# Optimization experiments

Hardware: AMD Instinct MI355X
Metric: run time of the kernel (lower is better)

Reference implementation:

```python
import jax, jax.numpy as jnp
import numpy as np

N, E, DIN, DH, DOUT, H, G = 50000, 640000, 128, 64, 64, 4, 16

_PARAM_SHAPES = {
    "gat1_W": (DIN, H * DH), "gat1_asrc": (H, DH), "gat1_adst": (H, DH), "gat1_b": (DH,),
    "gat2_W": (DH, H * DH), "gat2_asrc": (H, DH), "gat2_adst": (H, DH), "gat2_b": (DH,),
    "gin_W1": (DH, DH), "gin_b1": (DH,), "gin_W2": (DH, DH), "gin_b2": (DH,),
    "sage1_Wl": (DH, DH), "sage1_bl": (DH,), "sage1_Wr": (DH, DH),
    "sage2_Wl": (DH, DH), "sage2_bl": (DH,), "sage2_Wr": (DH, DH),
    "tr_Wq": (DH, H * DH), "tr_bq": (H * DH,), "tr_Wk": (DH, H * DH), "tr_bk": (H * DH,),
    "tr_Wv": (DH, H * DH), "tr_bv": (H * DH,), "tr_Ws": (DH, DH), "tr_bs": (DH,),
    "ec_W1": (2 * DH, DH), "ec_b1": (DH,), "ec_W2": (DH, DH), "ec_b2": (DH,),
    "fc1_W": (DH, DH), "fc1_b": (DH,), "fc2_W": (DH, DOUT), "fc2_b": (DOUT,),
}
_PARAM_NAMES = list(_PARAM_SHAPES)


def setup_inputs() -> dict:
    key = jax.random.key(0)
    inp = {}
    inp["x"] = jax.random.normal(jax.random.fold_in(key, 0), (N, DIN), jnp.float32)
    inp["edge_index"] = jax.random.randint(jax.random.fold_in(key, 1), (2, E), 0, N, dtype=jnp.int32)
    inp["batch"] = jnp.sort(jax.random.randint(jax.random.fold_in(key, 2), (N,), 0, G, dtype=jnp.int32))
    for i, (name, shp) in enumerate(_PARAM_SHAPES.items()):
        inp[name] = jax.random.normal(jax.random.fold_in(key, 10 + i), shp, jnp.float32) * 0.05
    return inp


def _edge_softmax(logit, dst, n):
    # softmax over incoming edges of each target node (PyG scatter-softmax)
    m = jax.ops.segment_max(logit, dst, num_segments=n)
    e = jnp.exp(logit - m[dst])
    z = jax.ops.segment_sum(e, dst, num_segments=n)
    return e / (z[dst] + 1e-16)


def _forward(x, src, dst, batch, p):
    relu = jax.nn.relu
    # GATConv adds self-loops by default
    loop = jnp.arange(N, dtype=src.dtype)
    src_sl = jnp.concatenate([src, loop])
    dst_sl = jnp.concatenate([dst, loop])

    def gat(h_in, W, a_s, a_d, b):
        h = (h_in @ W).reshape(N, H, DH)                    # [N,H,D]
        ls = jnp.einsum('nhd,hd->nh', h, a_s)
        ld = jnp.einsum('nhd,hd->nh', h, a_d)
        logit = jax.nn.leaky_relu(ls[src_sl] + ld[dst_sl], 0.2)   # [E+N,H]
        alpha = _edge_softmax(logit, dst_sl, N)
        out = jax.ops.segment_sum(h[src_sl] * alpha[:, :, None], dst_sl, num_segments=N)
        return out.mean(axis=1) + b                          # concat=False -> head mean + bias

    x1 = relu(gat(x, p["gat1_W"], p["gat1_asrc"], p["gat1_adst"], p["gat1_b"]))
    x2 = relu(gat(x1, p["gat2_W"], p["gat2_asrc"], p["gat2_adst"], p["gat2_b"]))

    # GINConv: nn((1+eps)*x + sum_j x_j), eps=0
    agg = jax.ops.segment_sum(x2[src], dst, num_segments=N)
    x3 = relu(relu((x2 + agg) @ p["gin_W1"] + p["gin_b1"]) @ p["gin_W2"] + p["gin_b2"])

    deg = jax.ops.segment_sum(jnp.ones((E,), x.dtype), dst, num_segments=N)
    deg = jnp.maximum(deg, 1.0)[:, None]

    def sage(h_in, Wl, bl, Wr):
        mean = jax.ops.segment_sum(h_in[src], dst, num_segments=N) / deg
        return mean @ Wl + bl + h_in @ Wr

    xs = relu(sage(x3, p["sage1_Wl"], p["sage1_bl"], p["sage1_Wr"]))
    x4 = relu(sage(xs, p["sage2_Wl"], p["sage2_bl"], p["sage2_Wr"]))

    # TransformerConv (heads=4, concat=False, root_weight skip)
    q = (x4 @ p["tr_Wq"] + p["tr_bq"]).reshape(N, H, DH)
    k = (x4 @ p["tr_Wk"] + p["tr_bk"]).reshape(N, H, DH)
    v = (x4 @ p["tr_Wv"] + p["tr_bv"]).reshape(N, H, DH)
    logit = (q[dst] * k[src]).sum(-1) * (1.0 / np.sqrt(DH))  # [E,H]
    alpha = _edge_softmax(logit, dst, N)
    tout = jax.ops.segment_sum(v[src] * alpha[:, :, None], dst, num_segments=N).mean(axis=1)
    x5 = relu(tout + x4 @ p["tr_Ws"] + p["tr_bs"])

    # EdgeConv: max_j nn([x_i, x_j - x_i])
    xi = x5[dst]
    feat = jnp.concatenate([xi, x5[src] - xi], axis=1)       # [E, 2*DH]
    msg = relu(feat @ p["ec_W1"] + p["ec_b1"]) @ p["ec_W2"] + p["ec_b2"]
    emax = jax.ops.segment_max(msg, dst, num_segments=N)
    x6 = relu(jnp.where(jnp.isfinite(emax), emax, 0.0))      # isolated nodes -> 0

    # global_mean_pool over batch ids
    cnt = jax.ops.segment_sum(jnp.ones((N,), x.dtype), batch, num_segments=G)
    gmean = jax.ops.segment_sum(x6, batch, num_segments=G) / jnp.maximum(cnt, 1.0)[:, None]

    # dropout layers are identity in eval mode
    return relu(gmean @ p["fc1_W"] + p["fc1_b"]) @ p["fc2_W"] + p["fc2_b"]


def reference(x, edge_index, batch,
              gat1_W, gat1_asrc, gat1_adst, gat1_b,
              gat2_W, gat2_asrc, gat2_adst, gat2_b,
              gin_W1, gin_b1, gin_W2, gin_b2,
              sage1_Wl, sage1_bl, sage1_Wr,
              sage2_Wl, sage2_bl, sage2_Wr,
              tr_Wq, tr_bq, tr_Wk, tr_bk, tr_Wv, tr_bv, tr_Ws, tr_bs,
              ec_W1, ec_b1, ec_W2, ec_b2,
              fc1_W, fc1_b, fc2_W, fc2_b):
    L = dict(locals())
    p = {n: L[n] for n in _PARAM_NAMES}
    return _forward(x, edge_index[0], edge_index[1], batch, p)
```

## Files before the change

### kernel.cpp

```cpp
#include <hip/hip_runtime.h>

#define NN 50000
#define EE 640000
#define GG 16
#define N64 (NN*64)

static inline int cdiv(int a,int b){return (a+b-1)/b;}

typedef __attribute__((ext_vector_type(8))) short bfrag;
typedef __attribute__((ext_vector_type(4))) float ffrag;
typedef __attribute__((ext_vector_type(2))) float f32x2;

__device__ __forceinline__ float lrelu(float x){ return x>0.f? x : 0.2f*x; }
__device__ __forceinline__ unsigned fenc(float f){
  unsigned u=__float_as_uint(f);
  return (u&0x80000000u)? ~u : (u|0x80000000u);
}
__device__ __forceinline__ float bf2f(unsigned short u){ return __uint_as_float(((unsigned)u)<<16); }
__device__ __forceinline__ unsigned short f2bf(float f){
  unsigned u=__float_as_uint(f);
  u += 0x7FFFu + ((u>>16)&1u);
  return (unsigned short)(u>>16);
}
__device__ __forceinline__ unsigned char f2f8(float f){
  return (unsigned char)(__builtin_amdgcn_cvt_pk_fp8_f32(f,f,0,false)&0xff);
}
__device__ __forceinline__ void f8x4(unsigned u, float& e0,float& e1,float& e2,float& e3){
  f32x2 lo=__builtin_amdgcn_cvt_pk_f32_fp8((int)u,false);
  f32x2 hi=__builtin_amdgcn_cvt_pk_f32_fp8((int)u,true);
  e0=lo.x; e1=lo.y; e2=hi.x; e3=hi.y;
}
__device__ __forceinline__ float dot4f8(unsigned a, unsigned b){
  f32x2 al=__builtin_amdgcn_cvt_pk_f32_fp8((int)a,false);
  f32x2 ah=__builtin_amdgcn_cvt_pk_f32_fp8((int)a,true);
  f32x2 bl=__builtin_amdgcn_cvt_pk_f32_fp8((int)b,false);
  f32x2 bh=__builtin_amdgcn_cvt_pk_f32_fp8((int)b,true);
  return al.x*bl.x+al.y*bl.y+ah.x*bh.x+ah.y*bh.y;
}

__global__ void zero_kernel(unsigned* p, int n){
  int i=blockIdx.x*blockDim.x+threadIdx.x;
  if(i<n) p[i]=0u;
}

__global__ void hist_kernel(const int* __restrict__ dst, int* __restrict__ cnt){
  int e=blockIdx.x*blockDim.x+threadIdx.x;
  if(e<EE) atomicAdd(&cnt[dst[e]],1);
}

__global__ __launch_bounds__(1024) void scan1_kernel(const int* __restrict__ cnt,
    int* __restrict__ rowptr, int* __restrict__ bsum){
  __shared__ int wsum[16];
  int t=threadIdx.x, b=blockIdx.x;
  int i=b*1024+t;
  int v=(i<NN)?cnt[i]:0;
  int lane=t&63, w=t>>6;
  int inc=v;
  #pragma unroll
  for(int o=1;o<64;o<<=1){ int u=__shfl_up(inc,o,64); if(lane>=o) inc+=u; }
  if(lane==63) wsum[w]=inc;
  __syncthreads();
  if(t<16){
    int s=wsum[t];
    #pragma unroll
    for(int o=1;o<16;o<<=1){ int u=__shfl_up(s,o,16); if(t>=o) s+=u; }
    wsum[t]=s;
  }
  __syncthreads();
  int woff=(w>0)?wsum[w-1]:0;
  if(i<NN) rowptr[i]=woff+inc-v;
  if(t==1023) bsum[b]=wsum[15];
}

__global__ void scan2_kernel(const int* __restrict__ bsum, int* __restrict__ boff, int* __restrict__ rowptr, int nb){
  int t=threadIdx.x;
  int v=(t<nb)?bsum[t]:0;
  int inc=v;
  #pragma unroll
  for(int o=1;o<64;o<<=1){ int u=__shfl_up(inc,o,64); if(t>=o) inc+=u; }
  if(t<nb) boff[t]=inc-v;
  if(t==63) rowptr[NN]=inc;
}

__global__ void scan3_kernel(int* __restrict__ rowptr, const int* __restrict__ boff,
                             const int* __restrict__ cnt, float* __restrict__ invdeg){
  int i=blockIdx.x*blockDim.x+threadIdx.x;
  if(i<NN){
    rowptr[i]+=boff[i>>10];
    invdeg[i]=1.f/fmaxf((float)cnt[i],1.f);
  }
}

__global__ void fill_kernel(const int* __restrict__ src, const int* __restrict__ dst,
                            const int* __restrict__ rowptr, int* __restrict__ fillp,
                            int* __restrict__ srcS, int* __restrict__ dstS){
  int e=blockIdx.x*blockDim.x+threadIdx.x;
  if(e>=EE) return;
  int d=dst[e];
  int p=rowptr[d]+atomicAdd(&fillp[d],1);
  srcS[p]=src[e]; dstS[p]=d;
}

__global__ void cvtx_kernel(const float* __restrict__ x, unsigned short* __restrict__ xb){
  int i=blockIdx.x*blockDim.x+threadIdx.x;
  if(i>=NN*32) return;
  float4 v=*(const float4*)(x+(size_t)i*4);
  ushort4 o; o.x=f2bf(v.x); o.y=f2bf(v.y); o.z=f2bf(v.z); o.w=f2bf(v.w);
  *(ushort4*)(xb+(size_t)i*4)=o;
}

__global__ void prep_kernel(
    const float* __restrict__ g1W, const float* __restrict__ g2W,
    const float* __restrict__ giW1, const float* __restrict__ giW2,
    const float* __restrict__ s1Wl, const float* __restrict__ s1Wr,
    const float* __restrict__ s2Wl, const float* __restrict__ s2Wr,
    const float* __restrict__ Wq, const float* __restrict__ Wk,
    const float* __restrict__ Wv, const float* __restrict__ Ws,
    const float* __restrict__ ecW1, const float* __restrict__ ecW2,
    const float* __restrict__ bq, const float* __restrict__ bk, const float* __restrict__ eb1,
    unsigned short* __restrict__ wt, float* __restrict__ bqk, float* __restrict__ bPQ){
  int i=blockIdx.x*blockDim.x+threadIdx.x;
  if(i<32768){ int n=i>>7,k=i&127; wt[i]=f2bf(g1W[k*256+n]); return; } i-=32768;
  if(i<16384){ int n=i>>6,k=i&63; wt[32768+i]=f2bf(g2W[k*256+n]); return; } i-=16384;
  if(i<4096){ int n=i>>6,k=i&63; wt[49152+i]=f2bf(giW1[k*64+n]); return; } i-=4096;
  if(i<4096){ int n=i>>6,k=i&63; wt[53248+i]=f2bf(giW2[k*64+n]); return; } i-=4096;
  if(i<8192){ int n=i>>7,k=i&127; float v=(k<64)?s1Wl[k*64+n]:s1Wr[(k-64)*64+n];
              wt[57344+i]=f2bf(v); return; } i-=8192;
  if(i<8192){ int n=i>>7,k=i&127; float v=(k<64)?s2Wl[k*64+n]:s2Wr[(k-64)*64+n];
              wt[65536+i]=f2bf(v); return; } i-=8192;
  if(i<32768){ int n=i>>6,k=i&63; float v=(n<256)?Wq[k*256+n]:Wk[k*256+(n-256)];
               wt[73728+i]=f2bf(v); return; } i-=32768;
  if(i<16384){ int n=i>>6,k=i&63; wt[106496+i]=f2bf(Wv[k*256+n]); return; } i-=16384;
  if(i<4096){ int n=i>>6,k=i&63; wt[122880+i]=f2bf(Ws[k*64+n]); return; } i-=4096;
  if(i<8192){ int n=i>>6,k=i&63;
              float v=(n<64)?(ecW1[k*64+n]-ecW1[(64+k)*64+n]):ecW1[(64+k)*64+(n-64)];
              wt[126976+i]=f2bf(v); return; } i-=8192;
  if(i<4096){ int n=i>>6,k=i&63; wt[135168+i]=f2bf(ecW2[k*64+n]); return; } i-=4096;
  if(i<640){
    if(i<256) bqk[i]=bq[i];
    else if(i<512) bqk[i]=bk[i-256];
    else { int j=i-512; bPQ[j]=(j<64)?eb1[j]:0.f; }
  }
}

template<int K>
__global__ __launch_bounds__(256) void mgemm_kernel(
    const unsigned short* __restrict__ A, const unsigned short* __restrict__ Wt,
    const float* __restrict__ bias,
    float* __restrict__ Cf, unsigned short* __restrict__ Cb, unsigned char* __restrict__ C8,
    int ldc, int relu_flag, int c8dh,
    const float* __restrict__ a_s, const float* __restrict__ a_d,
    float* __restrict__ lsO, float* __restrict__ ldO){
  __shared__ float lsP[2][4][64];
  const int m0=blockIdx.x*64;
  const int tid=threadIdx.x;
  const int w=tid>>6, l=tid&63, lo=l&15, quad=l>>4;
  const int colg=blockIdx.y*64 + w*16 + lo;
  const unsigned short* wrow=Wt+(size_t)colg*K+quad*8;
  ffrag acc[4];
  #pragma unroll
  for(int t=0;t<4;t++) acc[t]=(ffrag){0.f,0.f,0.f,0.f};
  int rows[4];
  #pragma unroll
  for(int t=0;t<4;t++){ int r=m0+t*16+lo; rows[t]=(r<NN)?r:(NN-1); }
  #pragma unroll
  for(int kc=0;kc<K;kc+=32){
    bfrag b=*(const bfrag*)(wrow+kc);
    #pragma unroll
    for(int t=0;t<4;t++){
      bfrag a=*(const bfrag*)(A+(size_t)rows[t]*K+kc+quad*8);
      acc[t]=__builtin_amdgcn_mfma_f32_16x16x32_bf16(a,b,acc[t],0,0,0);
    }
  }
  float bv=bias?bias[colg]:0.f;
  float asv=0.f,adv=0.f;
  if(lsO){ asv=a_s[colg]; adv=a_d[colg]; }
  #pragma unroll
  for(int t=0;t<4;t++){
    #pragma unroll
    for(int r=0;r<4;r++){
      float v=acc[t][r]+bv;
      if(relu_flag) v=fmaxf(v,0.f);
      int row=m0+t*16+quad*4+r;
      if(row<NN){
        if(C8){ int ci=c8dh?(((colg&63)<<2)|(colg>>6)):colg; C8[(size_t)row*ldc+ci]=f2f8(v); }
        else if(Cb) Cb[(size_t)row*ldc+colg]=f2bf(v);
        else   Cf[(size_t)row*ldc+colg]=v;
      }
      if(lsO){
        float ps=v*asv, pd=v*adv;
        #pragma unroll
        for(int o=1;o<16;o<<=1){ ps+=__shfl_xor(ps,o,16); pd+=__shfl_xor(pd,o,16); }
        if(lo==0){ int lr=t*16+quad*4+r; lsP[0][w][lr]=ps; lsP[1][w][lr]=pd; }
      }
    }
  }
  if(lsO){
    __syncthreads();
    if(tid<64){
      int row=m0+tid;
      if(row<NN){
        lsO[(size_t)row*4+blockIdx.y]=lsP[0][0][tid]+lsP[0][1][tid]+lsP[0][2][tid]+lsP[0][3][tid];
        ldO[(size_t)row*4+blockIdx.y]=lsP[1][0][tid]+lsP[1][1][tid]+lsP[1][2][tid]+lsP[1][3][tid];
      }
    }
  }
}

__global__ __launch_bounds__(256) void gat1p_kernel(const unsigned char* __restrict__ h8,
    const int* __restrict__ rowptr, const int* __restrict__ srcS,
    const float* __restrict__ ls4, const float* __restrict__ ld4,
    const float* __restrict__ bias, unsigned short* __restrict__ outb){
  __shared__ float cz[4][4];
  __shared__ float ca[4][4][64];
  int w=threadIdx.x>>6, lane=threadIdx.x&63;
  int n=blockIdx.x*2+(w>>1);
  int half=w&1;
  float z0=0.f,z1=0.f,z2=0.f,z3=0.f;
  float a0=0.f,a1=0.f,a2=0.f,a3=0.f;
  if(n<NN){
    const float4 ldv=*(const float4*)(ld4+(size_t)4*n);
    int r0=rowptr[n], r1=rowptr[n+1];
    int mid=(r0+r1)>>1;
    if(half==0){
      const float4 lsv=*(const float4*)(ls4+(size_t)4*n);
      z0=__expf(lrelu(lsv.x+ldv.x)); z1=__expf(lrelu(lsv.y+ldv.y));
      z2=__expf(lrelu(lsv.z+ldv.z)); z3=__expf(lrelu(lsv.w+ldv.w));
      float h0,h1,h2,h3;
      f8x4(*(const unsigned*)(h8+(size_t)n*256+lane*4),h0,h1,h2,h3);
      a0=z0*h0; a1=z1*h1; a2=z2*h2; a3=z3*h3;
    }
    int j = half? mid : r0;
    int je= half? r1  : mid;
    for(; j+3<je; j+=4){
      int s0=srcS[j], s1=srcS[j+1], s2=srcS[j+2], s3=srcS[j+3];
      float4 L0=*(const float4*)(ls4+(size_t)4*s0);
      float4 L1=*(const float4*)(ls4+(size_t)4*s1);
      float4 L2=*(const float4*)(ls4+(size_t)4*s2);
      float4 L3=*(const float4*)(ls4+(size_t)4*s3);
      unsigned u0=*(const unsigned*)(h8+(size_t)s0*256+lane*4);
      unsigned u1=*(const unsigned*)(h8+(size_t)s1*256+lane*4);
      unsigned u2=*(const unsigned*)(h8+(size_t)s2*256+lane*4);
      unsigned u3=*(const unsigned*)(h8+(size_t)s3*256+lane*4);
      float E0x=__expf(lrelu(L0.x+ldv.x)),E0y=__expf(lrelu(L0.y+ldv.y)),
            E0z=__expf(lrelu(L0.z+ldv.z)),E0w=__expf(lrelu(L0.w+ldv.w));
      float E1x=__expf(lrelu(L1.x+ldv.x)),E1y=__expf(lrelu(L1.y+ldv.y)),
            E1z=__expf(lrelu(L1.z+ldv.z)),E1w=__expf(lrelu(L1.w+ldv.w));
      float E2x=__expf(lrelu(L2.x+ldv.x)),E2y=__expf(lrelu(L2.y+ldv.y)),
            E2z=__expf(lrelu(L2.z+ldv.z)),E2w=__expf(lrelu(L2.w+ldv.w));
      float E3x=__expf(lrelu(L3.x+ldv.x)),E3y=__expf(lrelu(L3.y+ldv.y)),
            E3z=__expf(lrelu(L3.z+ldv.z)),E3w=__expf(lrelu(L3.w+ldv.w));
      float h00,h01,h02,h03; f8x4(u0,h00,h01,h02,h03);
      float h10,h11,h12,h13; f8x4(u1,h10,h11,h12,h13);
      float h20,h21,h22,h23; f8x4(u2,h20,h21,h22,h23);
      float h30,h31,h32,h33; f8x4(u3,h30,h31,h32,h33);
      z0+=(E0x+E1x)+(E2x+E3x); z1+=(E0y+E1y)+(E2y+E3y);
      z2+=(E0z+E1z)+(E2z+E3z); z3+=(E0w+E1w)+(E2w+E3w);
      a0+=(E0x*h00+E1x*h10)+(E2x*h20+E3x*h30);
      a1+=(E0y*h01+E1y*h11)+(E2y*h21+E3y*h31);
      a2+=(E0z*h02+E1z*h12)+(E2z*h22+E3z*h32);
      a3+=(E0w*h03+E1w*h13)+(E2w*h23+E3w*h33);
    }
    for(; j<je; j++){
      int s0=srcS[j];
      float4 L0=*(const float4*)(ls4+(size_t)4*s0);
      unsigned u0=*(const unsigned*)(h8+(size_t)s0*256+lane*4);
      float E0x=__expf(lrelu(L0.x+ldv.x)),E0y=__expf(lrelu(L0.y+ldv.y)),
            E0z=__expf(lrelu(L0.z+ldv.z)),E0w=__expf(lrelu(L0.w+ldv.w));
      float h00,h01,h02,h03; f8x4(u0,h00,h01,h02,h03);
      z0+=E0x; z1+=E0y; z2+=E0z; z3+=E0w;
      a0+=E0x*h00; a1+=E0y*h01; a2+=E0z*h02; a3+=E0w*h03;
    }
  }
  if(lane==0){ cz[w][0]=z0; cz[w][1]=z1; cz[w][2]=z2; cz[w][3]=z3; }
  ca[w][0][lane]=a0; ca[w][1][lane]=a1; ca[w][2][lane]=a2; ca[w][3][lane]=a3;
  __syncthreads();
  if(threadIdx.x<128){
    int ni=threadIdx.x>>6, l=threadIdx.x&63;
    int n2=blockIdx.x*2+ni;
    if(n2<NN){
      int w0=ni*2, w1=w0+1;
      float Z0=cz[w0][0]+cz[w1][0], Z1=cz[w0][1]+cz[w1][1];
      float Z2=cz[w0][2]+cz[w1][2], Z3=cz[w0][3]+cz[w1][3];
      float A0=ca[w0][0][l]+ca[w1][0][l], A1=ca[w0][1][l]+ca[w1][1][l];
      float A2=ca[w0][2][l]+ca[w1][2][l], A3=ca[w0][3][l]+ca[w1][3][l];
      float r=0.25f*(A0/(Z0+1e-16f)+A1/(Z1+1e-16f)+A2/(Z2+1e-16f)+A3/(Z3+1e-16f))+bias[l];
      outb[(size_t)n2*64+l]=f2bf(fmaxf(r,0.f));
    }
  }
}

__global__ __launch_bounds__(256) void agg_kernel(const unsigned short* __restrict__ xin,
    const int* __restrict__ rowptr, const int* __restrict__ srcS,
    unsigned short* __restrict__ out){
  int n=blockIdx.x*4+(threadIdx.x>>6);
  int lane=threadIdx.x&63;
  if(n>=NN) return;
  int r0=rowptr[n], r1=rowptr[n+1];
  float acc=bf2f(xin[(size_t)n*64+lane]);
  int j=r0;
  for(; j+3<r1; j+=4){
    int s0=srcS[j], s1=srcS[j+1], s2=srcS[j+2], s3=srcS[j+3];
    acc+=(bf2f(xin[(size_t)s0*64+lane])+bf2f(xin[(size_t)s1*64+lane]))
        +(bf2f(xin[(size_t)s2*64+lane])+bf2f(xin[(size_t)s3*64+lane]));
  }
  for(; j<r1; j++) acc+=bf2f(xin[(size_t)srcS[j]*64+lane]);
  out[(size_t)n*64+lane]=f2bf(acc);
}

__global__ __launch_bounds__(256) void agg2_kernel(const unsigned short* __restrict__ xin,
    const int* __restrict__ rowptr, const int* __restrict__ srcS,
    const float* __restrict__ invdeg, unsigned short* __restrict__ out128b){
  int n=blockIdx.x*4+(threadIdx.x>>6);
  int lane=threadIdx.x&63;
  if(n>=NN) return;
  int r0=rowptr[n], r1=rowptr[n+1];
  float acc=0.f;
  int j=r0;
  for(; j+3<r1; j+=4){
    int s0=srcS[j], s1=srcS[j+1], s2=srcS[j+2], s3=srcS[j+3];
    acc+=(bf2f(xin[(size_t)s0*64+lane])+bf2f(xin[(size_t)s1*64+lane]))
        +(bf2f(xin[(size_t)s2*64+lane])+bf2f(xin[(size_t)s3*64+lane]));
  }
  for(; j<r1; j++) acc+=bf2f(xin[(size_t)srcS[j]*64+lane]);
  out128b[(size_t)n*128+lane]=f2bf(acc*invdeg[n]);
  out128b[(size_t)n*128+64+lane]=xin[(size_t)n*64+lane];
}

__global__ __launch_bounds__(256) void tr_pass1_kernel(const int* __restrict__ srcS, const int* __restrict__ dstS,
    const unsigned char* __restrict__ qk8, float* __restrict__ lg){
  int e=blockIdx.x*16+(threadIdx.x>>4);
  int t=threadIdx.x&15;
  if(e>=EE) return;
  int s=srcS[e], d=dstS[e];
  const unsigned char* qd=qk8+(size_t)d*512+t*4;
  const unsigned char* ks=qk8+(size_t)s*512+256+t*4;
  unsigned ku0=*(const unsigned*)(ks);
  unsigned ku1=*(const unsigned*)(ks+64);
  unsigned ku2=*(const unsigned*)(ks+128);
  unsigned ku3=*(const unsigned*)(ks+192);
  unsigned qu0=*(const unsigned*)(qd);
  unsigned qu1=*(const unsigned*)(qd+64);
  unsigned qu2=*(const unsigned*)(qd+128);
  unsigned qu3=*(const unsigned*)(qd+192);
  float v0=dot4f8(ku0,qu0);
  float v1=dot4f8(ku1,qu1);
  float v2=dot4f8(ku2,qu2);
  float v3=dot4f8(ku3,qu3);
  #pragma unroll
  for(int o=1;o<16;o<<=1){
    v0+=__shfl_xor(v0,o,16); v1+=__shfl_xor(v1,o,16);
    v2+=__shfl_xor(v2,o,16); v3+=__shfl_xor(v3,o,16);
  }
  if(t==0)
    *(float4*)(lg+(size_t)4*e)=make_float4(__expf(v0*0.125f),__expf(v1*0.125f),
                                           __expf(v2*0.125f),__expf(v3*0.125f));
}

__global__ __launch_bounds__(256) void tr_pass2_kernel(const int* __restrict__ rowptr, const int* __restrict__ srcS,
    const float* __restrict__ lg,
    const unsigned char* __restrict__ v8, const float* __restrict__ skip, unsigned short* __restrict__ x5b){
  __shared__ float cz[4][4];
  __shared__ float ca[4][4][64];
  int w=threadIdx.x>>6, lane=threadIdx.x&63;
  int n=blockIdx.x*2+(w>>1);
  int half=w&1;
  float z0=0.f,z1=0.f,z2=0.f,z3=0.f;
  float a0=0.f,a1=0.f,a2=0.f,a3=0.f;
  if(n<NN){
    int r0=rowptr[n], r1=rowptr[n+1];
    int mid=(r0+r1)>>1;
    int j = half? mid : r0;
    int je= half? r1  : mid;
    for(; j+3<je; j+=4){
      int s0=srcS[j], s1=srcS[j+1], s2=srcS[j+2], s3=srcS[j+3];
      const float4 E0=*(const float4*)(lg+(size_t)4*j);
      const float4 E1=*(const float4*)(lg+(size_t)4*(j+1));
      const float4 E2=*(const float4*)(lg+(size_t)4*(j+2));
      const float4 E3=*(const float4*)(lg+(size_t)4*(j+3));
      unsigned u0=*(const unsigned*)(v8+(size_t)s0*256+lane*4);
      unsigned u1=*(const unsigned*)(v8+(size_t)s1*256+lane*4);
      unsigned u2=*(const unsigned*)(v8+(size_t)s2*256+lane*4);
      unsigned u3=*(const unsigned*)(v8+(size_t)s3*256+lane*4);
      float h00,h01,h02,h03; f8x4(u0,h00,h01,h02,h03);
      float h10,h11,h12,h13; f8x4(u1,h10,h11,h12,h13);
      float h20,h21,h22,h23; f8x4(u2,h20,h21,h22,h23);
      float h30,h31,h32,h33; f8x4(u3,h30,h31,h32,h33);
      z0+=(E0.x+E1.x)+(E2.x+E3.x); z1+=(E0.y+E1.y)+(E2.y+E3.y);
      z2+=(E0.z+E1.z)+(E2.z+E3.z); z3+=(E0.w+E1.w)+(E2.w+E3.w);
      a0+=(E0.x*h00+E1.x*h10)+(E2.x*h20+E3.x*h30);
      a1+=(E0.y*h01+E1.y*h11)+(E2.y*h21+E3.y*h31);
      a2+=(E0.z*h02+E1.z*h12)+(E2.z*h22+E3.z*h32);
      a3+=(E0.w*h03+E1.w*h13)+(E2.w*h23+E3.w*h33);
    }
    for(; j<je; j++){
      int s0=srcS[j];
      const float4 E0=*(const float4*)(lg+(size_t)4*j);
      unsigned u0=*(const unsigned*)(v8+(size_t)s0*256+lane*4);
      float h00,h01,h02,h03; f8x4(u0,h00,h01,h02,h03);
      z0+=E0.x; z1+=E0.y; z2+=E0.z; z3+=E0.w;
      a0+=E0.x*h00; a1+=E0.y*h01; a2+=E0.z*h02; a3+=E0.w*h03;
    }
  }
  if(lane==0){ cz[w][0]=z0; cz[w][1]=z1; cz[w][2]=z2; cz[w][3]=z3; }
  ca[w][0][lane]=a0; ca[w][1][lane]=a1; ca[w][2][lane]=a2; ca[w][3][lane]=a3;
  __syncthreads();
  if(threadIdx.x<128){
    int ni=threadIdx.x>>6, l=threadIdx.x&63;
    int n2=blockIdx.x*2+ni;
    if(n2<NN){
      int w0=ni*2, w1=w0+1;
      float Z0=cz[w0][0]+cz[w1][0], Z1=cz[w0][1]+cz[w1][1];
      float Z2=cz[w0][2]+cz[w1][2], Z3=cz[w0][3]+cz[w1][3];
      float A0=ca[w0][0][l]+ca[w1][0][l], A1=ca[w0][1][l]+ca[w1][1][l];
      float A2=ca[w0][2][l]+ca[w1][2][l], A3=ca[w0][3][l]+ca[w1][3][l];
      float t=0.25f*(A0/(Z0+1e-16f)+A1/(Z1+1e-16f)+A2/(Z2+1e-16f)+A3/(Z3+1e-16f))+skip[(size_t)n2*64+l];
      x5b[(size_t)n2*64+l]=f2bf(fmaxf(t,0.f));
    }
  }
}

__global__ __launch_bounds__(256) void edgeconv3_kernel(
    const unsigned short* __restrict__ PQ,
    const int* __restrict__ srcS, const int* __restrict__ dstS,
    const unsigned short* __restrict__ W2t, const float* __restrict__ b2,
    unsigned* __restrict__ emax){
  __shared__ unsigned short Hs[64][72];
  __shared__ float As[64][66];
  __shared__ int dstL[64];
  const int e0=blockIdx.x*64;
  const int tid=threadIdx.x;
  if(tid<64) dstL[tid]=dstS[e0+tid];
  #pragma unroll
  for(int it=0;it<4;it++){
    int linear=it*1024+tid*4;
    int m=linear>>6, k=linear&63;
    int e=e0+m;
    int dn=dstS[e], sn=srcS[e];
    ushort4 pu=*(const ushort4*)(PQ+(size_t)dn*128+k);
    ushort4 qu=*(const ushort4*)(PQ+(size_t)sn*128+64+k);
    ushort4 hh;
    hh.x=f2bf(fmaxf(bf2f(pu.x)+bf2f(qu.x),0.f));
    hh.y=f2bf(fmaxf(bf2f(pu.y)+bf2f(qu.y),0.f));
    hh.z=f2bf(fmaxf(bf2f(pu.z)+bf2f(qu.z),0.f));
    hh.w=f2bf(fmaxf(bf2f(pu.w)+bf2f(qu.w),0.f));
    *(ushort4*)&Hs[m][k]=hh;
  }
  __syncthreads();
  const int w=tid>>6, l=tid&63, lo=l&15, quad=l>>4;
  const int colg=w*16+lo;
  ffrag acc[4];
  #pragma unroll
  for(int t=0;t<4;t++) acc[t]=(ffrag){0.f,0.f,0.f,0.f};
  #pragma unroll
  for(int kc=0;kc<64;kc+=32){
    bfrag b=*(const bfrag*)(W2t+(size_t)colg*64+kc+quad*8);
    #pragma unroll
    for(int t=0;t<4;t++){
      bfrag a=*(const bfrag*)(&Hs[t*16+lo][kc+quad*8]);
      acc[t]=__builtin_amdgcn_mfma_f32_16x16x32_bf16(a,b,acc[t],0,0,0);
    }
  }
  float bv=b2[colg];
  #pragma unroll
  for(int t=0;t<4;t++)
    #pragma unroll
    for(int r=0;r<4;r++)
      As[t*16+quad*4+r][colg]=acc[t][r]+bv;
  __syncthreads();
  if(tid<64){
    const int c=tid;
    const int dFirst=dstL[0], dLast=dstL[63];
    int dprev=dFirst;
    float mx=As[0][c];
    #pragma unroll 8
    for(int m=1;m<64;m++){
      int dn=dstL[m];
      float v=As[m][c];
      if(dn!=dprev){
        unsigned* addr=&emax[(size_t)dprev*64+c];
        unsigned enc=fenc(mx);
        if(dprev!=dFirst && dprev!=dLast) *addr=enc;
        else atomicMax(addr,enc);
        dprev=dn; mx=v;
      }else mx=fmaxf(mx,v);
    }
    unsigned* addr=&emax[(size_t)dprev*64+c];
    unsigned enc=fenc(mx);
    if(dprev!=dFirst && dprev!=dLast) *addr=enc;
    else atomicMax(addr,enc);
  }
}

__global__ __launch_bounds__(256) void pool_kernel(const unsigned* __restrict__ emax, const int* __restrict__ batch,
                                                   float* __restrict__ pooled){
  const int NB=200;
  int base=blockIdx.x*NB;
  int lane=threadIdx.x&63;
  int wsub=threadIdx.x>>6;
  float acc=0.f; int curg=-1;
  for(int idx=wsub; idx<NB; idx+=4){
    int n=base+idx;
    if(n>=NN) break;
    int g=batch[n];
    if(g!=curg){
      if(curg>=0) atomicAdd(&pooled[curg*64+lane],acc);
      acc=0.f; curg=g;
    }
    unsigned u=emax[(size_t)n*64+lane];
    acc+=(u>=0x80000000u)? __uint_as_float(u&0x7fffffffu) : 0.f;
  }
  if(curg>=0) atomicAdd(&pooled[curg*64+lane],acc);
}

__global__ __launch_bounds__(256) void final_kernel(const float* __restrict__ pooled, const int* __restrict__ batch,
    const float* __restrict__ fc1W, const float* __restrict__ fc1b,
    const float* __restrict__ fc2W, const float* __restrict__ fc2b,
    float* __restrict__ out){
  __shared__ float gm[16][64];
  __shared__ float t1[16][64];
  __shared__ int cgs[17];
  int t=threadIdx.x;
  if(t<17){
    int lo=0, hi=NN;
    while(lo<hi){ int mid=(lo+hi)>>1; if(batch[mid]<t) lo=mid+1; else hi=mid; }
    cgs[t]=lo;
  }
  __syncthreads();
  for(int r=0;r<4;r++){
    int idx=r*256+t; int g=idx>>6, d=idx&63;
    float c=(float)(cgs[g+1]-cgs[g]);
    gm[g][d]=pooled[idx]/fmaxf(c,1.f);
  }
  __syncthreads();
  for(int r=0;r<4;r++){
    int idx=r*256+t; int g=idx>>6, d=idx&63;
    float a=fc1b[d];
    for(int k2=0;k2<64;k2++) a+=gm[g][k2]*fc1W[k2*64+d];
    t1[g][d]=fmaxf(a,0.f);
  }
  __syncthreads();
  for(int r=0;r<4;r++){
    int idx=r*256+t; int g=idx>>6, d=idx&63;
    float a=fc2b[d];
    for(int k2=0;k2<64;k2++) a+=t1[g][k2]*fc2W[k2*64+d];
    out[idx]=a;
  }
}

extern "C" void kernel_launch(void* const* d_in, const int* in_sizes, int n_in,
                              void* d_out, int out_size, void* d_ws, size_t ws_size,
                              hipStream_t stream){
  const float* x       =(const float*)d_in[0];
  const int*   ei      =(const int*)  d_in[1];
  const int*   src     =ei;
  const int*   dst     =ei+EE;
  const int*   batch   =(const int*)  d_in[2];
  const float* gat1_W  =(const float*)d_in[3];
  const float* gat1_as =(const float*)d_in[4];
  const float* gat1_ad =(const float*)d_in[5];
  const float* gat1_b  =(const float*)d_in[6];
  const float* gat2_W  =(const float*)d_in[7];
  const float* gat2_as =(const float*)d_in[8];
  const float* gat2_ad =(const float*)d_in[9];
  const float* gat2_b  =(const float*)d_in[10];
  const float* gin_W1  =(const float*)d_in[11];
  const float* gin_b1  =(const float*)d_in[12];
  const float* gin_W2  =(const float*)d_in[13];
  const float* gin_b2  =(const float*)d_in[14];
  const float* sage1_Wl=(const float*)d_in[15];
  const float* sage1_bl=(const float*)d_in[16];
  const float* sage1_Wr=(const float*)d_in[17];
  const float* sage2_Wl=(const float*)d_in[18];
  const float* sage2_bl=(const float*)d_in[19];
  const float* sage2_Wr=(const float*)d_in[20];
  const float* tr_Wq   =(const float*)d_in[21];
  const float* tr_bq   =(const float*)d_in[22];
  const float* tr_Wk   =(const float*)d_in[23];
  const float* tr_bk   =(const float*)d_in[24];
  const float* tr_Wv   =(const float*)d_in[25];
  const float* tr_bv   =(const float*)d_in[26];
  const float* tr_Ws   =(const float*)d_in[27];
  const float* tr_bs   =(const float*)d_in[28];
  const float* ec_W1   =(const float*)d_in[29];
  const float* ec_b1   =(const float*)d_in[30];
  const float* ec_W2   =(const float*)d_in[31];
  const float* ec_b2   =(const float*)d_in[32];
  const float* fc1_W   =(const float*)d_in[33];
  const float* fc1_b   =(const float*)d_in[34];
  const float* fc2_W   =(const float*)d_in[35];
  const float* fc2_b   =(const float*)d_in[36];

  float* base=(float*)d_ws;
  size_t off=0;
  auto alloc=[&](size_t n){ float* p=base+off; off+=n; return p; };
  float* A_big =alloc((size_t)NN*256);
  float* nb0   =alloc(N64);
  float* nb1   =alloc(N64);
  float* nb2   =alloc(N64);
  float* nb3   =alloc(N64);
  float* nb4   =alloc(N64);
  float* nb5   =alloc(N64);
  float* logitE=alloc((size_t)EE*4);
  float* ls    =alloc(NN*4);
  float* ldb   =alloc(NN*4);
  float* invdeg=alloc(NN);
  float* pooled=alloc(GG*64);
  float* wbuf  =alloc(70000);
  float* bbuf  =alloc(640);
  int* ibase=(int*)(base+off);
  int* srcS  =ibase;
  int* dstS  =ibase+EE;
  int* cnt   =ibase+2*EE;
  int* fillp =ibase+2*EE+NN;
  int* rowptr=ibase+2*EE+2*NN;
  int* bsum  =ibase+2*EE+3*NN+8;
  int* boff  =bsum+64;

  const int BT=256;
  const int NSB=cdiv(NN,1024);
  zero_kernel<<<cdiv(2*NN,BT),BT,0,stream>>>((unsigned*)cnt,2*NN);
  zero_kernel<<<cdiv(GG*64,BT),BT,0,stream>>>((unsigned*)pooled,GG*64);
  zero_kernel<<<cdiv(N64,BT),BT,0,stream>>>((unsigned*)nb5,N64);
  hist_kernel<<<cdiv(EE,BT),BT,0,stream>>>(dst,cnt);
  scan1_kernel<<<NSB,1024,0,stream>>>(cnt,rowptr,bsum);
  scan2_kernel<<<1,64,0,stream>>>(bsum,boff,rowptr,NSB);
  scan3_kernel<<<cdiv(NN,BT),BT,0,stream>>>(rowptr,boff,cnt,invdeg);
  fill_kernel<<<cdiv(EE,BT),BT,0,stream>>>(src,dst,rowptr,fillp,srcS,dstS);

  const int GB=cdiv(NN,64);
  const int GW=cdiv(NN,4);
  const int GW2=cdiv(NN,2);

  unsigned short* wt =(unsigned short*)wbuf;
  float* bqk=bbuf;
  float* bPQ=bbuf+512;
  unsigned char*  h8   =(unsigned char*)A_big;
  unsigned char*  qk8  =(unsigned char*)A_big;
  unsigned short* xb   =(unsigned short*)A_big+(size_t)NN*256;
  unsigned short* xcatb=(unsigned short*)A_big;
  unsigned short* x1b  =(unsigned short*)nb0;
  unsigned short* x2b  =(unsigned short*)nb1;
  unsigned short* tb   =(unsigned short*)nb2;
  unsigned short* hb3  =(unsigned short*)nb3;
  unsigned short* x3b  =(unsigned short*)nb1;
  unsigned short* xsb  =(unsigned short*)nb2;
  unsigned short* x4b  =(unsigned short*)nb0;
  unsigned char*  v8   =(unsigned char*)nb1;
  unsigned short* x5b  =(unsigned short*)nb4;
  float* skipf=nb3;
  unsigned short* PQb  =(unsigned short*)nb1;

  prep_kernel<<<cdiv(139904,BT),BT,0,stream>>>(gat1_W,gat2_W,gin_W1,gin_W2,
      sage1_Wl,sage1_Wr,sage2_Wl,sage2_Wr,tr_Wq,tr_Wk,tr_Wv,tr_Ws,ec_W1,ec_W2,
      tr_bq,tr_bk,ec_b1,wt,bqk,bPQ);
  cvtx_kernel<<<cdiv(NN*32,BT),BT,0,stream>>>(x,xb);

  mgemm_kernel<128><<<dim3(GB,4),BT,0,stream>>>(xb,wt,nullptr,nullptr,nullptr,h8,256,0,1,
                                                gat1_as,gat1_ad,ls,ldb);
  gat1p_kernel<<<GW2,BT,0,stream>>>(h8,rowptr,srcS,ls,ldb,gat1_b,x1b);
  mgemm_kernel<64><<<dim3(GB,4),BT,0,stream>>>(x1b,wt+32768,nullptr,nullptr,nullptr,h8,256,0,1,
                                               gat2_as,gat2_ad,ls,ldb);
  gat1p_kernel<<<GW2,BT,0,stream>>>(h8,rowptr,srcS,ls,ldb,gat2_b,x2b);
  agg_kernel<<<GW,BT,0,stream>>>(x2b,rowptr,srcS,tb);
  mgemm_kernel<64><<<dim3(GB,1),BT,0,stream>>>(tb,wt+49152,gin_b1,nullptr,hb3,nullptr,64,1,0,
                                               nullptr,nullptr,nullptr,nullptr);
  mgemm_kernel<64><<<dim3(GB,1),BT,0,stream>>>(hb3,wt+53248,gin_b2,nullptr,x3b,nullptr,64,1,0,
                                               nullptr,nullptr,nullptr,nullptr);
  agg2_kernel<<<GW,BT,0,stream>>>(x3b,rowptr,srcS,invdeg,xcatb);
  mgemm_kernel<128><<<dim3(GB,1),BT,0,stream>>>(xcatb,wt+57344,sage1_bl,nullptr,xsb,nullptr,64,1,0,
                                                nullptr,nullptr,nullptr,nullptr);
  agg2_kernel<<<GW,BT,0,stream>>>(xsb,rowptr,srcS,invdeg,xcatb);
  mgemm_kernel<128><<<dim3(GB,1),BT,0,stream>>>(xcatb,wt+65536,sage2_bl,nullptr,x4b,nullptr,64,1,0,
                                                nullptr,nullptr,nullptr,nullptr);
  mgemm_kernel<64><<<dim3(GB,8),BT,0,stream>>>(x4b,wt+73728,bqk,nullptr,nullptr,qk8,512,0,0,
                                               nullptr,nullptr,nullptr,nullptr);
  tr_pass1_kernel<<<cdiv(EE,16),BT,0,stream>>>(srcS,dstS,qk8,logitE);
  mgemm_kernel<64><<<dim3(GB,4),BT,0,stream>>>(x4b,wt+106496,tr_bv,nullptr,nullptr,v8,256,0,1,
                                               nullptr,nullptr,nullptr,nullptr);
  mgemm_kernel<64><<<dim3(GB,1),BT,0,stream>>>(x4b,wt+122880,tr_bs,skipf,nullptr,nullptr,64,0,0,
                                               nullptr,nullptr,nullptr,nullptr);
  tr_pass2_kernel<<<GW2,BT,0,stream>>>(rowptr,srcS,logitE,v8,skipf,x5b);
  mgemm_kernel<64><<<dim3(GB,2),BT,0,stream>>>(x5b,wt+126976,bPQ,nullptr,PQb,nullptr,128,0,0,
                                               nullptr,nullptr,nullptr,nullptr);
  edgeconv3_kernel<<<EE/64,BT,0,stream>>>(PQb,srcS,dstS,wt+135168,ec_b2,(unsigned*)nb5);
  pool_kernel<<<cdiv(NN,200),BT,0,stream>>>((unsigned*)nb5,batch,pooled);
  final_kernel<<<1,BT,0,stream>>>(pooled,batch,fc1_W,fc1_b,fc2_W,fc2_b,(float*)d_out);
}
```

Before: 821.4 us.

## Gather neighbor features in fp8 and precompute GAT edge exponentials

Producers of gathered activations (GAT2 output, GIN output, SAGE1 output, EdgeConv P/Q) now also write an fp8 copy. The aggregation and edgeconv kernels gather that fp8 copy instead of bf16, which halves the bytes per random neighbor read. A new per-edge kernel precomputes the GAT attention exponentials once, so the aggregation loop streams them instead of gathering source logits and computing exp. The costs are extra write traffic, an extra launch plus an edge-sized buffer for each GAT layer, and lower accuracy in the aggregated sums.

```diff
diff --git a/kernel.cpp b/kernel.cpp
--- a/kernel.cpp
+++ b/kernel.cpp
@@ -29,6 +29,10 @@
   f32x2 lo=__builtin_amdgcn_cvt_pk_f32_fp8((int)u,false);
   f32x2 hi=__builtin_amdgcn_cvt_pk_f32_fp8((int)u,true);
   e0=lo.x; e1=lo.y; e2=hi.x; e3=hi.y;
+}
+__device__ __forceinline__ float f8one(unsigned b){
+  f32x2 lo=__builtin_amdgcn_cvt_pk_f32_fp8((int)b,false);
+  return lo.x;
 }
 __device__ __forceinline__ float dot4f8(unsigned a, unsigned b){
   f32x2 al=__builtin_amdgcn_cvt_pk_f32_fp8((int)a,false);
@@ -148,7 +152,7 @@
     const unsigned short* __restrict__ A, const unsigned short* __restrict__ Wt,
     const float* __restrict__ bias,
     float* __restrict__ Cf, unsigned short* __restrict__ Cb, unsigned char* __restrict__ C8,
-    int ldc, int relu_flag, int c8dh,
+    int ldc, int relu_flag, int c8mode,
     const float* __restrict__ a_s, const float* __restrict__ a_d,
     float* __restrict__ lsO, float* __restrict__ ldO){
   __shared__ float lsP[2][4][64];
@@ -183,9 +187,15 @@
       if(relu_flag) v=fmaxf(v,0.f);
       int row=m0+t*16+quad*4+r;
       if(row<NN){
-        if(C8){ int ci=c8dh?(((colg&63)<<2)|(colg>>6)):colg; C8[(size_t)row*ldc+ci]=f2f8(v); }
-        else if(Cb) Cb[(size_t)row*ldc+colg]=f2bf(v);
-        else   Cf[(size_t)row*ldc+colg]=v;
+        if(Cf) Cf[(size_t)row*ldc+colg]=v;
+        if(Cb) Cb[(size_t)row*ldc+colg]=f2bf(v);
+        if(C8){
+          size_t idx;
+          if(c8mode==1)      idx=(size_t)row*ldc + (((colg&63)<<2)|(colg>>6));
+          else if(c8mode==2) idx=(size_t)((colg<64)?0:N64) + (size_t)row*64 + (colg&63);
+          else               idx=(size_t)row*ldc + colg;
+          C8[idx]=f2f8(v);
+        }
       }
       if(lsO){
         float ps=v*asv, pd=v*adv;
@@ -207,10 +217,24 @@
   }
 }
 
+__global__ void gat_exp_kernel(const int* __restrict__ srcS, const int* __restrict__ dstS,
+    const float* __restrict__ ls4, const float* __restrict__ ld4, float* __restrict__ eE){
+  int j=blockIdx.x*blockDim.x+threadIdx.x;
+  if(j>=EE) return;
+  int s=srcS[j], d=dstS[j];
+  const float4 a=*(const float4*)(ls4+(size_t)4*s);
+  const float4 b=*(const float4*)(ld4+(size_t)4*d);
+  *(float4*)(eE+(size_t)4*j)=make_float4(
+    __expf(lrelu(a.x+b.x)),__expf(lrelu(a.y+b.y)),
+    __expf(lrelu(a.z+b.z)),__expf(lrelu(a.w+b.w)));
+}
+
 __global__ __launch_bounds__(256) void gat1p_kernel(const unsigned char* __restrict__ h8,
     const int* __restrict__ rowptr, const int* __restrict__ srcS,
+    const float* __restrict__ eE,
     const float* __restrict__ ls4, const float* __restrict__ ld4,
-    const float* __restrict__ bias, unsigned short* __restrict__ outb){
+    const float* __restrict__ bias, unsigned short* __restrict__ outb,
+    unsigned char* __restrict__ out8){
   __shared__ float cz[4][4];
   __shared__ float ca[4][4][64];
   int w=threadIdx.x>>6, lane=threadIdx.x&63;
@@ -219,10 +243,10 @@
   float z0=0.f,z1=0.f,z2=0.f,z3=0.f;
   float a0=0.f,a1=0.f,a2=0.f,a3=0.f;
   if(n<NN){
-    const float4 ldv=*(const float4*)(ld4+(size_t)4*n);
     int r0=rowptr[n], r1=rowptr[n+1];
     int mid=(r0+r1)>>1;
     if(half==0){
+      const float4 ldv=*(const float4*)(ld4+(size_t)4*n);
       const float4 lsv=*(const float4*)(ls4+(size_t)4*n);
       z0=__expf(lrelu(lsv.x+ldv.x)); z1=__expf(lrelu(lsv.y+ldv.y));
       z2=__expf(lrelu(lsv.z+ldv.z)); z3=__expf(lrelu(lsv.w+ldv.w));
@@ -234,42 +258,32 @@
     int je= half? r1  : mid;
     for(; j+3<je; j+=4){
       int s0=srcS[j], s1=srcS[j+1], s2=srcS[j+2], s3=srcS[j+3];
-      float4 L0=*(const float4*)(ls4+(size_t)4*s0);
-      float4 L1=*(const float4*)(ls4+(size_t)4*s1);
-      float4 L2=*(const float4*)(ls4+(size_t)4*s2);
-      float4 L3=*(const float4*)(ls4+(size_t)4*s3);
+      const float4 E0=*(const float4*)(eE+(size_t)4*j);
+      const float4 E1=*(const float4*)(eE+(size_t)4*(j+1));
+      const float4 E2=*(const float4*)(eE+(size_t)4*(j+2));
+      const float4 E3=*(const float4*)(eE+(size_t)4*(j+3));
       unsigned u0=*(const unsigned*)(h8+(size_t)s0*256+lane*4);
       unsigned u1=*(const unsigned*)(h8+(size_t)s1*256+lane*4);
       unsigned u2=*(const unsigned*)(h8+(size_t)s2*256+lane*4);
       unsigned u3=*(const unsigned*)(h8+(size_t)s3*256+lane*4);
-      float E0x=__expf(lrelu(L0.x+ldv.x)),E0y=__expf(lrelu(L0.y+ldv.y)),
-            E0z=__expf(lrelu(L0.z+ldv.z)),E0w=__expf(lrelu(L0.w+ldv.w));
-      float E1x=__expf(lrelu(L1.x+ldv.x)),E1y=__expf(lrelu(L1.y+ldv.y)),
-            E1z=__expf(lrelu(L1.z+ldv.z)),E1w=__expf(lrelu(L1.w+ldv.w));
-      float E2x=__expf(lrelu(L2.x+ldv.x)),E2y=__expf(lrelu(L2.y+ldv.y)),
-            E2z=__expf(lrelu(L2.z+ldv.z)),E2w=__expf(lrelu(L2.w+ldv.w));
-      float E3x=__expf(lrelu(L3.x+ldv.x)),E3y=__expf(lrelu(L3.y+ldv.y)),
-            E3z=__expf(lrelu(L3.z+ldv.z)),E3w=__expf(lrelu(L3.w+ldv.w));
       float h00,h01,h02,h03; f8x4(u0,h00,h01,h02,h03);
       float h10,h11,h12,h13; f8x4(u1,h10,h11,h12,h13);
       float h20,h21,h22,h23; f8x4(u2,h20,h21,h22,h23);
       float h30,h31,h32,h33; f8x4(u3,h30,h31,h32,h33);
-      z0+=(E0x+E1x)+(E2x+E3x); z1+=(E0y+E1y)+(E2y+E3y);
-      z2+=(E0z+E1z)+(E2z+E3z); z3+=(E0w+E1w)+(E2w+E3w);
-      a0+=(E0x*h00+E1x*h10)+(E2x*h20+E3x*h30);
-      a1+=(E0y*h01+E1y*h11)+(E2y*h21+E3y*h31);
-      a2+=(E0z*h02+E1z*h12)+(E2z*h22+E3z*h32);
-      a3+=(E0w*h03+E1w*h13)+(E2w*h23+E3w*h33);
+      z0+=(E0.x+E1.x)+(E2.x+E3.x); z1+=(E0.y+E1.y)+(E2.y+E3.y);
+      z2+=(E0.z+E1.z)+(E2.z+E3.z); z3+=(E0.w+E1.w)+(E2.w+E3.w);
+      a0+=(E0.x*h00+E1.x*h10)+(E2.x*h20+E3.x*h30);
+      a1+=(E0.y*h01+E1.y*h11)+(E2.y*h21+E3.y*h31);
+      a2+=(E0.z*h02+E1.z*h12)+(E2.z*h22+E3.z*h32);
+      a3+=(E0.w*h03+E1.w*h13)+(E2.w*h23+E3.w*h33);
     }
     for(; j<je; j++){
       int s0=srcS[j];
-      float4 L0=*(const float4*)(ls4+(size_t)4*s0);
+      const float4 E0=*(const float4*)(eE+(size_t)4*j);
       unsigned u0=*(const unsigned*)(h8+(size_t)s0*256+lane*4);
-      float E0x=__expf(lrelu(L0.x+ldv.x)),E0y=__expf(lrelu(L0.y+ldv.y)),
-            E0z=__expf(lrelu(L0.z+ldv.z)),E0w=__expf(lrelu(L0.w+ldv.w));
       float h00,h01,h02,h03; f8x4(u0,h00,h01,h02,h03);
-      z0+=E0x; z1+=E0y; z2+=E0z; z3+=E0w;
-      a0+=E0x*h00; a1+=E0y*h01; a2+=E0z*h02; a3+=E0w*h03;
+      z0+=E0.x; z1+=E0.y; z2+=E0.z; z3+=E0.w;
+      a0+=E0.x*h00; a1+=E0.y*h01; a2+=E0.z*h02; a3+=E0.w*h03;
     }
   }
   if(lane==0){ cz[w][0]=z0; cz[w][1]=z1; cz[w][2]=z2; cz[w][3]=z3; }
@@ -285,12 +299,15 @@
       float A0=ca[w0][0][l]+ca[w1][0][l], A1=ca[w0][1][l]+ca[w1][1][l];
       float A2=ca[w0][2][l]+ca[w1][2][l], A3=ca[w0][3][l]+ca[w1][3][l];
       float r=0.25f*(A0/(Z0+1e-16f)+A1/(Z1+1e-16f)+A2/(Z2+1e-16f)+A3/(Z3+1e-16f))+bias[l];
-      outb[(size_t)n2*64+l]=f2bf(fmaxf(r,0.f));
+      float rr=fmaxf(r,0.f);
+      outb[(size_t)n2*64+l]=f2bf(rr);
+      if(out8) out8[(size_t)n2*64+l]=f2f8(rr);
     }
   }
 }
 
 __global__ __launch_bounds__(256) void agg_kernel(const unsigned short* __restrict__ xin,
+    const unsigned char* __restrict__ xin8,
     const int* __restrict__ rowptr, const int* __restrict__ srcS,
     unsigned short* __restrict__ out){
   int n=blockIdx.x*4+(threadIdx.x>>6);
@@ -301,14 +318,18 @@
   int j=r0;
   for(; j+3<r1; j+=4){
     int s0=srcS[j], s1=srcS[j+1], s2=srcS[j+2], s3=srcS[j+3];
-    acc+=(bf2f(xin[(size_t)s0*64+lane])+bf2f(xin[(size_t)s1*64+lane]))
-        +(bf2f(xin[(size_t)s2*64+lane])+bf2f(xin[(size_t)s3*64+lane]));
-  }
-  for(; j<r1; j++) acc+=bf2f(xin[(size_t)srcS[j]*64+lane]);
+    unsigned b0=xin8[(size_t)s0*64+lane];
+    unsigned b1=xin8[(size_t)s1*64+lane];
+    unsigned b2=xin8[(size_t)s2*64+lane];
+    unsigned b3=xin8[(size_t)s3*64+lane];
+    acc+=(f8one(b0)+f8one(b1))+(f8one(b2)+f8one(b3));
+  }
+  for(; j<r1; j++) acc+=f8one(xin8[(size_t)srcS[j]*64+lane]);
   out[(size_t)n*64+lane]=f2bf(acc);
 }
 
 __global__ __launch_bounds__(256) void agg2_kernel(const unsigned short* __restrict__ xin,
+    const unsigned char* __restrict__ xin8,
     const int* __restrict__ rowptr, const int* __restrict__ srcS,
     const float* __restrict__ invdeg, unsigned short* __restrict__ out128b){
   int n=blockIdx.x*4+(threadIdx.x>>6);
@@ -319,10 +340,13 @@
   int j=r0;
   for(; j+3<r1; j+=4){
     int s0=srcS[j], s1=srcS[j+1], s2=srcS[j+2], s3=srcS[j+3];
-    acc+=(bf2f(xin[(size_t)s0*64+lane])+bf2f(xin[(size_t)s1*64+lane]))
-        +(bf2f(xin[(size_t)s2*64+lane])+bf2f(xin[(size_t)s3*64+lane]));
-  }
-  for(; j<r1; j++) acc+=bf2f(xin[(size_t)srcS[j]*64+lane]);
+    unsigned b0=xin8[(size_t)s0*64+lane];
+    unsigned b1=xin8[(size_t)s1*64+lane];
+    unsigned b2=xin8[(size_t)s2*64+lane];
+    unsigned b3=xin8[(size_t)s3*64+lane];
+    acc+=(f8one(b0)+f8one(b1))+(f8one(b2)+f8one(b3));
+  }
+  for(; j<r1; j++) acc+=f8one(xin8[(size_t)srcS[j]*64+lane]);
   out128b[(size_t)n*128+lane]=f2bf(acc*invdeg[n]);
   out128b[(size_t)n*128+64+lane]=xin[(size_t)n*64+lane];
 }
@@ -421,13 +445,15 @@
 }
 
 __global__ __launch_bounds__(256) void edgeconv3_kernel(
-    const unsigned short* __restrict__ PQ,
+    const unsigned char* __restrict__ PQ8,
     const int* __restrict__ srcS, const int* __restrict__ dstS,
     const unsigned short* __restrict__ W2t, const float* __restrict__ b2,
     unsigned* __restrict__ emax){
   __shared__ unsigned short Hs[64][72];
   __shared__ float As[64][66];
   __shared__ int dstL[64];
+  const unsigned char* P8=PQ8;
+  const unsigned char* Q8=PQ8+(size_t)N64;
   const int e0=blockIdx.x*64;
   const int tid=threadIdx.x;
   if(tid<64) dstL[tid]=dstS[e0+tid];
@@ -437,13 +463,15 @@
     int m=linear>>6, k=linear&63;
     int e=e0+m;
     int dn=dstS[e], sn=srcS[e];
-    ushort4 pu=*(const ushort4*)(PQ+(size_t)dn*128+k);
-    ushort4 qu=*(const ushort4*)(PQ+(size_t)sn*128+64+k);
+    unsigned pu=*(const unsigned*)(P8+(size_t)dn*64+k);
+    unsigned qu=*(const unsigned*)(Q8+(size_t)sn*64+k);
+    float p0,p1,p2,p3; f8x4(pu,p0,p1,p2,p3);
+    float q0,q1,q2,q3; f8x4(qu,q0,q1,q2,q3);
     ushort4 hh;
-    hh.x=f2bf(fmaxf(bf2f(pu.x)+bf2f(qu.x),0.f));
-    hh.y=f2bf(fmaxf(bf2f(pu.y)+bf2f(qu.y),0.f));
-    hh.z=f2bf(fmaxf(bf2f(pu.z)+bf2f(qu.z),0.f));
-    hh.w=f2bf(fmaxf(bf2f(pu.w)+bf2f(qu.w),0.f));
+    hh.x=f2bf(fmaxf(p0+q0,0.f));
+    hh.y=f2bf(fmaxf(p1+q1,0.f));
+    hh.z=f2bf(fmaxf(p2+q2,0.f));
+    hh.w=f2bf(fmaxf(p3+q3,0.f));
     *(ushort4*)&Hs[m][k]=hh;
   }
   __syncthreads();
@@ -635,9 +663,14 @@
   unsigned short* wt =(unsigned short*)wbuf;
   float* bqk=bbuf;
   float* bPQ=bbuf+512;
-  unsigned char*  h8   =(unsigned char*)A_big;
-  unsigned char*  qk8  =(unsigned char*)A_big;
+  unsigned char*  Abc  =(unsigned char*)A_big;
+  unsigned char*  h8   =Abc;
+  unsigned char*  qk8  =Abc;
+  unsigned char*  PQ8  =Abc;
   unsigned short* xb   =(unsigned short*)A_big+(size_t)NN*256;
+  unsigned char*  x2f8 =Abc+26000000;
+  unsigned char*  x3f8 =Abc+30000000;
+  unsigned char*  xsf8 =Abc+34000000;
   unsigned short* xcatb=(unsigned short*)A_big;
   unsigned short* x1b  =(unsigned short*)nb0;
   unsigned short* x2b  =(unsigned short*)nb1;
@@ -649,7 +682,6 @@
   unsigned char*  v8   =(unsigned char*)nb1;
   unsigned short* x5b  =(unsigned short*)nb4;
   float* skipf=nb3;
-  unsigned short* PQb  =(unsigned short*)nb1;
 
   prep_kernel<<<cdiv(139904,BT),BT,0,stream>>>(gat1_W,gat2_W,gin_W1,gin_W2,
       sage1_Wl,sage1_Wr,sage2_Wl,sage2_Wr,tr_Wq,tr_Wk,tr_Wv,tr_Ws,ec_W1,ec_W2,
@@ -658,19 +690,21 @@
 
   mgemm_kernel<128><<<dim3(GB,4),BT,0,stream>>>(xb,wt,nullptr,nullptr,nullptr,h8,256,0,1,
                                                 gat1_as,gat1_ad,ls,ldb);
-  gat1p_kernel<<<GW2,BT,0,stream>>>(h8,rowptr,srcS,ls,ldb,gat1_b,x1b);
+  gat_exp_kernel<<<cdiv(EE,BT),BT,0,stream>>>(srcS,dstS,ls,ldb,logitE);
+  gat1p_kernel<<<GW2,BT,0,stream>>>(h8,rowptr,srcS,logitE,ls,ldb,gat1_b,x1b,nullptr);
   mgemm_kernel<64><<<dim3(GB,4),BT,0,stream>>>(x1b,wt+32768,nullptr,nullptr,nullptr,h8,256,0,1,
                                                gat2_as,gat2_ad,ls,ldb);
-  gat1p_kernel<<<GW2,BT,0,stream>>>(h8,rowptr,srcS,ls,ldb,gat2_b,x2b);
-  agg_kernel<<<GW,BT,0,stream>>>(x2b,rowptr,srcS,tb);
+  gat_exp_kernel<<<cdiv(EE,BT),BT,0,stream>>>(srcS,dstS,ls,ldb,logitE);
+  gat1p_kernel<<<GW2,BT,0,stream>>>(h8,rowptr,srcS,logitE,ls,ldb,gat2_b,x2b,x2f8);
+  agg_kernel<<<GW,BT,0,stream>>>(x2b,x2f8,rowptr,srcS,tb);
   mgemm_kernel<64><<<dim3(GB,1),BT,0,stream>>>(tb,wt+49152,gin_b1,nullptr,hb3,nullptr,64,1,0,
                                                nullptr,nullptr,nullptr,nullptr);
-  mgemm_kernel<64><<<dim3(GB,1),BT,0,stream>>>(hb3,wt+53248,gin_b2,nullptr,x3b,nullptr,64,1,0,
+  mgemm_kernel<64><<<dim3(GB,1),BT,0,stream>>>(hb3,wt+53248,gin_b2,nullptr,x3b,x3f8,64,1,0,
                                                nullptr,nullptr,nullptr,nullptr);
-  agg2_kernel<<<GW,BT,0,stream>>>(x3b,rowptr,srcS,invdeg,xcatb);
-  mgemm_kernel<128><<<dim3(GB,1),BT,0,stream>>>(xcatb,wt+57344,sage1_bl,nullptr,xsb,nullptr,64,1,0,
+  agg2_kernel<<<GW,BT,0,stream>>>(x3b,x3f8,rowptr,srcS,invdeg,xcatb);
+  mgemm_kernel<128><<<dim3(GB,1),BT,0,stream>>>(xcatb,wt+57344,sage1_bl,nullptr,xsb,xsf8,64,1,0,
                                                 nullptr,nullptr,nullptr,nullptr);
-  agg2_kernel<<<GW,BT,0,stream>>>(xsb,rowptr,srcS,invdeg,xcatb);
+  agg2_kernel<<<GW,BT,0,stream>>>(xsb,xsf8,rowptr,srcS,invdeg,xcatb);
   mgemm_kernel<128><<<dim3(GB,1),BT,0,stream>>>(xcatb,wt+65536,sage2_bl,nullptr,x4b,nullptr,64,1,0,
                                                 nullptr,nullptr,nullptr,nullptr);
   mgemm_kernel<64><<<dim3(GB,8),BT,0,stream>>>(x4b,wt+73728,bqk,nullptr,nullptr,qk8,512,0,0,
@@ -681,9 +715,9 @@
   mgemm_kernel<64><<<dim3(GB,1),BT,0,stream>>>(x4b,wt+122880,tr_bs,skipf,nullptr,nullptr,64,0,0,
                                                nullptr,nullptr,nullptr,nullptr);
   tr_pass2_kernel<<<GW2,BT,0,stream>>>(rowptr,srcS,logitE,v8,skipf,x5b);
-  mgemm_kernel<64><<<dim3(GB,2),BT,0,stream>>>(x5b,wt+126976,bPQ,nullptr,PQb,nullptr,128,0,0,
+  mgemm_kernel<64><<<dim3(GB,2),BT,0,stream>>>(x5b,wt+126976,bPQ,nullptr,nullptr,PQ8,64,0,2,
                                                nullptr,nullptr,nullptr,nullptr);
-  edgeconv3_kernel<<<EE/64,BT,0,stream>>>(PQb,srcS,dstS,wt+135168,ec_b2,(unsigned*)nb5);
+  edgeconv3_kernel<<<EE/64,BT,0,stream>>>(PQ8,srcS,dstS,wt+135168,ec_b2,(unsigned*)nb5);
   pool_kernel<<<cdiv(NN,200),BT,0,stream>>>((unsigned*)nb5,batch,pooled);
   final_kernel<<<1,BT,0,stream>>>(pooled,batch,fc1_W,fc1_b,fc2_W,fc2_b,(float*)d_out);
 }
```

New measurement: 816.8 us. Within noise of the previous version (-0.6%).
